# Optimization experiments

Hardware: AMD Instinct MI355X
Metric: run time of the kernel (lower is better)

The kernel has to match this reference:

```python
import jax, jax.numpy as jnp
import numpy as np

B, N, D, C, H = 8, 2048, 768, 2048, 3072
ROPE_BASE = 10000.0


def rms_norm(x, scale, eps=1e-6):
    x32 = x.astype(jnp.float32)
    normed = x32 * jax.lax.rsqrt(jnp.mean(x32 * x32, axis=-1, keepdims=True) + eps)
    return normed.astype(x.dtype) * scale


def apply_rope(x, pos):
    # x: [..., T, D], pos: [..., T] int. Half-split (llama-style) rotary embedding.
    half = x.shape[-1] // 2
    inv_freq = 1.0 / (ROPE_BASE ** (jnp.arange(half, dtype=jnp.float32) / half))
    ang = pos.astype(jnp.float32)[..., None] * inv_freq  # [..., T, half]
    cos, sin = jnp.cos(ang), jnp.sin(ang)
    x1, x2 = x[..., :half], x[..., half:]
    return jnp.concatenate([x1 * cos - x2 * sin, x1 * sin + x2 * cos], axis=-1)


def setup_inputs() -> dict:
    key = jax.random.key(0)
    ks = jax.random.split(key, 12)
    inp = {
        "latents": jax.random.normal(ks[0], (B, N, D), dtype=jnp.float32),
        "tau": jnp.float32(1.0),
        "residual_scaling": jnp.float32(1.0),
        "gumbel_noise_scale": jnp.float32(0.5),
        "positions": jnp.sort(jax.random.randint(ks[1], (B, max(N, C)), 0, 2048), axis=-1),
        # learned parameters (torch Linear weights stored [out, in])
        "codebook": jax.random.normal(ks[2], (C, D), dtype=jnp.float32),
        "norm_context_scale": jnp.ones((D,), jnp.float32),
        "norm_queries_scale": jnp.ones((D,), jnp.float32),
        "norm_ff_scale": jnp.ones((D,), jnp.float32),
        "Wq": jax.random.normal(ks[3], (D, D), jnp.float32) / np.sqrt(D),
        "Wk": jax.random.normal(ks[4], (D, D), jnp.float32) / np.sqrt(D),
        "Wv": jax.random.normal(ks[5], (D, D), jnp.float32) / np.sqrt(D),
        "bv": jnp.zeros((D,), jnp.float32),
        "Wc": jax.random.normal(ks[6], (D, D), jnp.float32) / np.sqrt(D),
        "W1": jax.random.normal(ks[7], (H, D), jnp.float32) / np.sqrt(D),
        "W2": jax.random.normal(ks[8], (D, H), jnp.float32) / np.sqrt(H),
        "W3": jax.random.normal(ks[9], (H, D), jnp.float32) / np.sqrt(D),
    }
    return inp


def reference(latents, tau, residual_scaling, gumbel_noise_scale, positions,
              codebook, norm_context_scale, norm_queries_scale, norm_ff_scale,
              Wq, Wk, Wv, bv, Wc, W1, W2, W3):
    scale = jnp.sqrt(jnp.float32(D))
    normed_context = rms_norm(codebook, norm_context_scale)        # [C, D]
    normed_queries = rms_norm(latents, norm_queries_scale)         # [B, N, D]

    q = jnp.einsum('bnd,ed->bne', normed_queries, Wq)              # [B, N, D]
    k = normed_context @ Wk.T                                      # [C, D]
    v = normed_context @ Wv.T + bv                                 # [C, D]

    q = apply_rope(q, positions[:, :N])                            # [B, N, D]
    k = apply_rope(jnp.broadcast_to(k, (B, C, D)), positions[:, :C])  # [B, C, D]

    log_alpha = jnp.einsum('bnd,bcd->bnc', q, k) / scale           # [B, N, C]

    u = jax.random.uniform(jax.random.key(42), log_alpha.shape, dtype=jnp.float32)
    gumbel = -jnp.log(-jnp.log(u + 1e-10) + 1e-10)
    log_alpha_tau = (log_alpha + gumbel_noise_scale * gumbel) / tau
    z = jax.nn.softmax(log_alpha_tau, axis=-1)                     # [B, N, C]

    attn = jnp.einsum('bnc,cd->bnd', z, v)                         # [B, N, D]
    y = jnp.einsum('bnd,ed->bne', attn, Wc)
    attn_output = residual_scaling * latents + y

    h = rms_norm(attn_output, norm_ff_scale)
    ff = jnp.einsum('bnh,dh->bnd', jax.nn.silu(jnp.einsum('bnd,hd->bnh', h, W1)) * jnp.einsum('bnd,hd->bnh', h, W3), W2)
    codebook_output = attn_output + ff
    return (codebook_output, log_alpha, log_alpha_tau, z)
```

## Files before the change

kernel.cpp:

```cpp
#include <hip/hip_runtime.h>
#include <cstdint>
#include <cstddef>


typedef __bf16 bf16_t;
typedef __bf16 bf16x8 __attribute__((ext_vector_type(8)));
typedef float  f32x4  __attribute__((ext_vector_type(4)));
typedef float  f32x16 __attribute__((ext_vector_type(16)));

#define B_    8
#define N_    2048
#define D_    768
#define C_    2048
#define H_    3072
#define NROWS 16384

#define WQ_OFF 0
#define WK_OFF 589824
#define WV_OFF 1179648
#define WC_OFF 1769472
#define W1_OFF 2359296
#define W3_OFF 4718592
#define W2_OFF 7077888
#define WTOT   9437184

#define WS_W     0ull
#define WS_TRIG  18874368ull
#define WS_VCT   25165824ull
#define WS_NC    28311552ull
#define WS_NQ    31457280ull
#define WS_Z     56623104ull
#define WS_H     28311552ull
#define WS_G     157286400ull
#define WS_VB    257949696ull

#define DO_CB    0ull
#define DO_LA    50331648ull
#define DO_LAT   184549376ull
#define DO_Z     318767104ull
#define DO_QBASE 184549376ull
#define DO_KBASE (184549376ull + 50331648ull)
#define DO_QROPE (234881024ull + 6291456ull)
#define DO_KROPE (241172480ull + 25165824ull)

__device__ __forceinline__ void gl_lds16(const void* g, void* l) {
  __builtin_amdgcn_global_load_lds((__attribute__((address_space(1))) void*)(g),
                                   (__attribute__((address_space(3))) void*)(l),
                                   16, 0, 0);
}

__device__ __forceinline__ void block_sync() {
  __builtin_amdgcn_sched_barrier(0);
  asm volatile("" ::: "memory");
  __builtin_amdgcn_s_barrier();
  asm volatile("" ::: "memory");
  __builtin_amdgcn_sched_barrier(0);
}

__device__ __forceinline__ uint32_t rotl32(uint32_t v, int d) {
  return (v << d) | (v >> (32 - d));
}
__device__ __forceinline__ void tf_round(uint32_t& x0, uint32_t& x1, int r) {
  x0 += x1; x1 = rotl32(x1, r); x1 ^= x0;
}
__device__ __forceinline__ uint2 threefry2x32(uint32_t k0, uint32_t k1,
                                              uint32_t x0, uint32_t x1) {
  const uint32_t k2 = k0 ^ k1 ^ 0x1BD11BDAu;
  x0 += k0; x1 += k1;
  tf_round(x0,x1,13); tf_round(x0,x1,15); tf_round(x0,x1,26); tf_round(x0,x1,6);
  x0 += k1; x1 += k2 + 1u;
  tf_round(x0,x1,17); tf_round(x0,x1,29); tf_round(x0,x1,16); tf_round(x0,x1,24);
  x0 += k2; x1 += k0 + 2u;
  tf_round(x0,x1,13); tf_round(x0,x1,15); tf_round(x0,x1,26); tf_round(x0,x1,6);
  x0 += k0; x1 += k1 + 3u;
  tf_round(x0,x1,17); tf_round(x0,x1,29); tf_round(x0,x1,16); tf_round(x0,x1,24);
  x0 += k1; x1 += k2 + 4u;
  tf_round(x0,x1,13); tf_round(x0,x1,15); tf_round(x0,x1,26); tf_round(x0,x1,6);
  x0 += k2; x1 += k0 + 5u;
  return make_uint2(x0, x1);
}

#define SWZ(o) ((o) ^ ((((o) >> 7) & 3) << 4))

#define PHASE_MFMA_OPEN() do { \
    block_sync(); \
    asm volatile("s_waitcnt lgkmcnt(0)" ::: "memory"); \
    __builtin_amdgcn_sched_barrier(0); \
    __builtin_amdgcn_s_setprio(1); \
  } while (0)
#define PHASE_MFMA_CLOSE() do { \
    __builtin_amdgcn_s_setprio(0); \
    __builtin_amdgcn_sched_barrier(0); \
  } while (0)

#define ROWMAP32(rg, kg) (((rg) & 3) + 8 * ((rg) >> 2) + 4 * (kg))

template <int EPI>
__global__ __launch_bounds__(512, 2) void gemm8p(
    const bf16_t* __restrict__ A, const bf16_t* __restrict__ B,
    void* outp, const void* auxp, const float* sptr,
    int M, int N, int K, long sA, long sB, long sO)
{
  __shared__ bf16_t As[2][2][8192];
  __shared__ bf16_t Bs[2][2][8192];
  const int tid  = threadIdx.x;
  const int lane = tid & 63;
  const int wid  = tid >> 6;
  const int wm = wid >> 2, wn = wid & 3;
  const int l31 = lane & 31, kg = lane >> 5;

  const int lin = (blockIdx.z * gridDim.y + blockIdx.y) * gridDim.x + blockIdx.x;
  const int swzb = (lin & 7) * 64 + (lin >> 3);
  const int bz = swzb >> 6;
  const int ny = (swzb & 63) >> 3;
  const int nx = swzb & 7;

  const bf16_t* Ab = A + (size_t)bz * (size_t)sA;
  const bf16_t* Bb = B + (size_t)bz * (size_t)sB;
  const int tm = ny * 256;
  const int tn = nx * 256;
  const int nt = K >> 6;

  const bf16_t *srcA0, *srcA1, *srcB0, *srcB1;
  {
    const int d0 = wid * 1024 + lane * 16;
    const int p0 = SWZ(d0);
    srcA0 = Ab + (size_t)(tm + (p0 >> 6)) * K + ((p0 & 63) >> 1);
    srcB0 = Bb + (size_t)(tn + (p0 >> 6)) * K + ((p0 & 63) >> 1);
    const int d1 = 8192 + wid * 1024 + lane * 16;
    const int p1 = SWZ(d1);
    srcA1 = Ab + (size_t)(tm + (p1 >> 6)) * K + ((p1 & 63) >> 1);
    srcB1 = Bb + (size_t)(tn + (p1 >> 6)) * K + ((p1 & 63) >> 1);
  }
  bf16_t* dstA = &As[0][0][0] + wid * 512;
  bf16_t* dstB = &Bs[0][0][0] + wid * 512;

  int olA[4][2], olB[2][2];
  #pragma unroll
  for (int mb = 0; mb < 4; ++mb)
    #pragma unroll
    for (int u = 0; u < 2; ++u) {
      const int o = ((wm * 128 + mb * 32 + l31) << 6) + u * 32 + (kg << 4);
      olA[mb][u] = SWZ(o);
    }
  #pragma unroll
  for (int nb = 0; nb < 2; ++nb)
    #pragma unroll
    for (int u = 0; u < 2; ++u) {
      const int o = ((wn * 64 + nb * 32 + l31) << 6) + u * 32 + (kg << 4);
      olB[nb][u] = SWZ(o);
    }

#define STG_A(tile_, kk_) do { \
    const size_t ko_ = (size_t)(tile_) * 64 + (size_t)(kk_) * 32; \
    bf16_t* db_ = dstA + (((tile_) & 1) ? 16384 : 0) + ((kk_) ? 8192 : 0); \
    gl_lds16(srcA0 + ko_, db_); \
    gl_lds16(srcA1 + ko_, db_ + 4096); \
  } while (0)
#define STG_B(tile_, kk_) do { \
    const size_t ko_ = (size_t)(tile_) * 64 + (size_t)(kk_) * 32; \
    bf16_t* db_ = dstB + (((tile_) & 1) ? 16384 : 0) + ((kk_) ? 8192 : 0); \
    gl_lds16(srcB0 + ko_, db_); \
    gl_lds16(srcB1 + ko_, db_ + 4096); \
  } while (0)

  f32x16 acc[4][2] = {};

  STG_A(0, 0); STG_B(0, 0); STG_A(0, 1); STG_B(0, 1);
  STG_B(1, 0); STG_A(1, 0); STG_B(1, 1);
  asm volatile("s_waitcnt vmcnt(6)" ::: "memory");
  block_sync();

  for (int t = 0; t < nt; ++t) {
    const int s = t & 1;
    bf16x8 bfr[2][2];
    #pragma unroll
    for (int q = 0; q < 4; ++q) {
      const int kk = q >> 1, mh = q & 1;
      if (q == 0)      { if (t + 1 < nt) STG_A(t + 1, 1); }
      else if (q == 1) { if (t + 2 < nt) STG_B(t + 2, 0); }
      else if (q == 2) { if (t + 2 < nt) STG_A(t + 2, 0); }
      else             { if (t + 2 < nt) STG_B(t + 2, 1); }
      if (mh == 0) {
        const char* Bbase = (const char*)&Bs[s][kk][0];
        #pragma unroll
        for (int nb = 0; nb < 2; ++nb)
          #pragma unroll
          for (int u = 0; u < 2; ++u)
            bfr[nb][u] = *(const bf16x8*)(Bbase + olB[nb][u]);
      }
      const char* Abase = (const char*)&As[s][kk][0];
      bf16x8 af[2][2];
      #pragma unroll
      for (int j = 0; j < 2; ++j)
        #pragma unroll
        for (int u = 0; u < 2; ++u)
          af[j][u] = *(const bf16x8*)(Abase + olA[mh * 2 + j][u]);
      PHASE_MFMA_OPEN();
      #pragma unroll
      for (int u = 0; u < 2; ++u)
        #pragma unroll
        for (int j = 0; j < 2; ++j)
          #pragma unroll
          for (int nb = 0; nb < 2; ++nb)
            acc[mh * 2 + j][nb] =
              __builtin_amdgcn_mfma_f32_32x32x16_bf16(af[j][u], bfr[nb][u], acc[mh * 2 + j][nb], 0, 0, 0);
      PHASE_MFMA_CLOSE();
      if (q == 3) asm volatile("s_waitcnt vmcnt(6)" ::: "memory");
      block_sync();
    }
  }
#undef STG_A
#undef STG_B

  #pragma unroll
  for (int mb = 0; mb < 4; ++mb) {
    #pragma unroll
    for (int nb = 0; nb < 2; ++nb) {
      const int cg = tn + wn * 64 + nb * 32 + l31;
      #pragma unroll
      for (int rg = 0; rg < 16; ++rg) {
        const int r = tm + wm * 128 + mb * 32 + ROWMAP32(rg, kg);
        const float v = acc[mb][nb][rg];
        const size_t idx = (size_t)r * N + cg;
        if (EPI == 1) {
          ((float*)outp)[(size_t)bz * sO + idx] = v * 0.03608439182435161f;
        } else {
          ((float*)outp)[(size_t)bz * sO + idx] = v;
        }
      }
    }
  }
}

template <int EPI>
__global__ __launch_bounds__(512, 2) void gemm_n384(
    const bf16_t* __restrict__ A, const bf16_t* __restrict__ B,
    void* outp, const void* auxp, const float* sptr, int K)
{
  __shared__ bf16_t As[2][2][4096];
  __shared__ bf16_t Bs[2][2][12288];
  const int tid  = threadIdx.x;
  const int lane = tid & 63;
  const int wid  = tid >> 6;
  const int wm = wid >> 2, wn = wid & 3;
  const int l31 = lane & 31, kg = lane >> 5;

  const int lin = blockIdx.y * 2 + blockIdx.x;
  const int swzb = (lin & 7) * 32 + (lin >> 3);
  const int ny = swzb >> 1;
  const int nx = swzb & 1;

  const int tm = ny * 128;
  const int tn = nx * 384;
  const int nt = K >> 6;

  const bf16_t *srcA, *srcB0, *srcB1, *srcB2;
  {
    const int d = wid * 1024 + lane * 16;
    const int p = SWZ(d);
    srcA = A + (size_t)(tm + (p >> 6)) * K + ((p & 63) >> 1);
    srcB0 = B + (size_t)(tn + (p >> 6)) * K + ((p & 63) >> 1);
    const int d1 = 8192 + d, p1 = SWZ(d1);
    srcB1 = B + (size_t)(tn + (p1 >> 6)) * K + ((p1 & 63) >> 1);
    const int d2 = 16384 + d, p2 = SWZ(d2);
    srcB2 = B + (size_t)(tn + (p2 >> 6)) * K + ((p2 & 63) >> 1);
  }
  bf16_t* dstA = &As[0][0][0] + wid * 512;
  bf16_t* dstB = &Bs[0][0][0] + wid * 512;

  int olA[2][2], olB[3][2];
  #pragma unroll
  for (int mb = 0; mb < 2; ++mb)
    #pragma unroll
    for (int u = 0; u < 2; ++u) {
      const int o = ((wm * 64 + mb * 32 + l31) << 6) + u * 32 + (kg << 4);
      olA[mb][u] = SWZ(o);
    }
  #pragma unroll
  for (int nb = 0; nb < 3; ++nb)
    #pragma unroll
    for (int u = 0; u < 2; ++u) {
      const int o = ((wn * 96 + nb * 32 + l31) << 6) + u * 32 + (kg << 4);
      olB[nb][u] = SWZ(o);
    }

#define STG_A(tile_, kk_) do { \
    const size_t ko_ = (size_t)(tile_) * 64 + (size_t)(kk_) * 32; \
    gl_lds16(srcA + ko_, dstA + (((tile_) & 1) ? 8192 : 0) + ((kk_) ? 4096 : 0)); \
  } while (0)
#define STG_B(tile_, kk_) do { \
    const size_t ko_ = (size_t)(tile_) * 64 + (size_t)(kk_) * 32; \
    bf16_t* db_ = dstB + (((tile_) & 1) ? 24576 : 0) + ((kk_) ? 12288 : 0); \
    gl_lds16(srcB0 + ko_, db_); \
    gl_lds16(srcB1 + ko_, db_ + 4096); \
    gl_lds16(srcB2 + ko_, db_ + 8192); \
  } while (0)

  f32x16 acc[2][3] = {};

  STG_A(0, 0); STG_B(0, 0); STG_A(0, 1); STG_B(0, 1);
  STG_B(1, 0); STG_A(1, 0); STG_B(1, 1);
  asm volatile("s_waitcnt vmcnt(7)" ::: "memory");
  block_sync();

  for (int t = 0; t < nt; ++t) {
    const int s = t & 1;
    bf16x8 bfr[3][2];
    #pragma unroll
    for (int q = 0; q < 4; ++q) {
      const int kk = q >> 1, mh = q & 1;
      if (q == 0)      { if (t + 1 < nt) STG_A(t + 1, 1); }
      else if (q == 1) { if (t + 2 < nt) STG_B(t + 2, 0); }
      else if (q == 2) { if (t + 2 < nt) STG_A(t + 2, 0); }
      else             { if (t + 2 < nt) STG_B(t + 2, 1); }
      if (mh == 0) {
        const char* Bbase = (const char*)&Bs[s][kk][0];
        #pragma unroll
        for (int nb = 0; nb < 3; ++nb)
          #pragma unroll
          for (int u = 0; u < 2; ++u)
            bfr[nb][u] = *(const bf16x8*)(Bbase + olB[nb][u]);
      }
      const char* Abase = (const char*)&As[s][kk][0];
      bf16x8 af[2];
      #pragma unroll
      for (int u = 0; u < 2; ++u)
        af[u] = *(const bf16x8*)(Abase + olA[mh][u]);
      PHASE_MFMA_OPEN();
      #pragma unroll
      for (int u = 0; u < 2; ++u)
        #pragma unroll
        for (int nb = 0; nb < 3; ++nb)
          acc[mh][nb] =
            __builtin_amdgcn_mfma_f32_32x32x16_bf16(af[u], bfr[nb][u], acc[mh][nb], 0, 0, 0);
      PHASE_MFMA_CLOSE();
      if (q == 3) asm volatile("s_waitcnt vmcnt(7)" ::: "memory");
      block_sync();
    }
  }
#undef STG_A
#undef STG_B

  const float sval = (EPI == 5) ? sptr[0] : 0.0f;
  #pragma unroll
  for (int mb = 0; mb < 2; ++mb) {
    #pragma unroll
    for (int nb = 0; nb < 3; ++nb) {
      const int cg = tn + wn * 96 + nb * 32 + l31;
      #pragma unroll
      for (int rg = 0; rg < 16; ++rg) {
        const int r = tm + wm * 64 + mb * 32 + ROWMAP32(rg, kg);
        const float v = acc[mb][nb][rg];
        const size_t idx = (size_t)r * 768 + cg;
        if (EPI == 2) {
          ((bf16_t*)outp)[idx] = (bf16_t)v;
        } else if (EPI == 5) {
          ((float*)outp)[idx] = sval * ((const float*)auxp)[idx] + v;
        } else {
          ((float*)outp)[idx] = ((const float*)auxp)[idx] + v;
        }
      }
    }
  }
}

__global__ __launch_bounds__(512, 2) void gemm_ff13(
    const bf16_t* __restrict__ A, const bf16_t* __restrict__ B1,
    const bf16_t* __restrict__ B3, bf16_t* __restrict__ G, int K)
{
  __shared__ bf16_t As[2][2][8192];
  __shared__ bf16_t B1s[2][2][4096];
  __shared__ bf16_t B3s[2][2][4096];
  const int tid  = threadIdx.x;
  const int lane = tid & 63;
  const int wid  = tid >> 6;
  const int wm = wid >> 2, wn = wid & 3;
  const int l31 = lane & 31, kg = lane >> 5;

  const int lin = blockIdx.y * 24 + blockIdx.x;
  const int swzb = (lin & 7) * 192 + (lin >> 3);
  const int cj = swzb / 192;
  const int local = swzb - cj * 192;
  const int st = local / 24;
  const int r  = local - st * 24;
  const int nx = cj * 3 + (r % 3);
  const int ny = st * 8 + (r / 3);

  const int tm = ny * 256;
  const int tn = nx * 128;
  const int nt = K >> 6;

  const bf16_t *srcA0, *srcA1, *srcB1p, *srcB3p;
  {
    const int d0 = wid * 1024 + lane * 16;
    const int p0 = SWZ(d0);
    srcA0 = A + (size_t)(tm + (p0 >> 6)) * K + ((p0 & 63) >> 1);
    srcB1p = B1 + (size_t)(tn + (p0 >> 6)) * K + ((p0 & 63) >> 1);
    srcB3p = B3 + (size_t)(tn + (p0 >> 6)) * K + ((p0 & 63) >> 1);
    const int d1 = 8192 + d0, p1 = SWZ(d1);
    srcA1 = A + (size_t)(tm + (p1 >> 6)) * K + ((p1 & 63) >> 1);
  }
  bf16_t* dstA  = &As[0][0][0]  + wid * 512;
  bf16_t* dstB1 = &B1s[0][0][0] + wid * 512;
  bf16_t* dstB3 = &B3s[0][0][0] + wid * 512;

  int olA[4][2], olB[2];
  #pragma unroll
  for (int mb = 0; mb < 4; ++mb)
    #pragma unroll
    for (int u = 0; u < 2; ++u) {
      const int o = ((wm * 128 + mb * 32 + l31) << 6) + u * 32 + (kg << 4);
      olA[mb][u] = SWZ(o);
    }
  #pragma unroll
  for (int u = 0; u < 2; ++u) {
    const int o = ((wn * 32 + l31) << 6) + u * 32 + (kg << 4);
    olB[u] = SWZ(o);
  }

#define STG_A(tile_, kk_) do { \
    const size_t ko_ = (size_t)(tile_) * 64 + (size_t)(kk_) * 32; \
    bf16_t* db_ = dstA + (((tile_) & 1) ? 16384 : 0) + ((kk_) ? 8192 : 0); \
    gl_lds16(srcA0 + ko_, db_); \
    gl_lds16(srcA1 + ko_, db_ + 4096); \
  } while (0)
#define STG_B(tile_, kk_) do { \
    const size_t ko_ = (size_t)(tile_) * 64 + (size_t)(kk_) * 32; \
    const int ro_ = (((tile_) & 1) ? 8192 : 0) + ((kk_) ? 4096 : 0); \
    gl_lds16(srcB1p + ko_, dstB1 + ro_); \
    gl_lds16(srcB3p + ko_, dstB3 + ro_); \
  } while (0)

  f32x16 acc1[4] = {};
  f32x16 acc3[4] = {};

  STG_A(0, 0); STG_B(0, 0); STG_A(0, 1); STG_B(0, 1);
  STG_B(1, 0); STG_A(1, 0); STG_B(1, 1);
  asm volatile("s_waitcnt vmcnt(6)" ::: "memory");
  block_sync();

  for (int t = 0; t < nt; ++t) {
    const int s = t & 1;
    bf16x8 b1r[2], b3r[2];
    #pragma unroll
    for (int q = 0; q < 4; ++q) {
      const int kk = q >> 1, mh = q & 1;
      if (q == 0)      { if (t + 1 < nt) STG_A(t + 1, 1); }
      else if (q == 1) { if (t + 2 < nt) STG_B(t + 2, 0); }
      else if (q == 2) { if (t + 2 < nt) STG_A(t + 2, 0); }
      else             { if (t + 2 < nt) STG_B(t + 2, 1); }
      if (mh == 0) {
        const char* B1base = (const char*)&B1s[s][kk][0];
        const char* B3base = (const char*)&B3s[s][kk][0];
        #pragma unroll
        for (int u = 0; u < 2; ++u) {
          b1r[u] = *(const bf16x8*)(B1base + olB[u]);
          b3r[u] = *(const bf16x8*)(B3base + olB[u]);
        }
      }
      const char* Abase = (const char*)&As[s][kk][0];
      bf16x8 af[2][2];
      #pragma unroll
      for (int j = 0; j < 2; ++j)
        #pragma unroll
        for (int u = 0; u < 2; ++u)
          af[j][u] = *(const bf16x8*)(Abase + olA[mh * 2 + j][u]);
      PHASE_MFMA_OPEN();
      #pragma unroll
      for (int u = 0; u < 2; ++u)
        #pragma unroll
        for (int j = 0; j < 2; ++j) {
          acc1[mh * 2 + j] =
            __builtin_amdgcn_mfma_f32_32x32x16_bf16(af[j][u], b1r[u], acc1[mh * 2 + j], 0, 0, 0);
          acc3[mh * 2 + j] =
            __builtin_amdgcn_mfma_f32_32x32x16_bf16(af[j][u], b3r[u], acc3[mh * 2 + j], 0, 0, 0);
        }
      PHASE_MFMA_CLOSE();
      if (q == 3) asm volatile("s_waitcnt vmcnt(6)" ::: "memory");
      block_sync();
    }
  }
#undef STG_A
#undef STG_B

  #pragma unroll
  for (int mb = 0; mb < 4; ++mb) {
    const int cg = tn + wn * 32 + l31;
    #pragma unroll
    for (int rg = 0; rg < 16; ++rg) {
      const int r2 = tm + wm * 128 + mb * 32 + ROWMAP32(rg, kg);
      const float f1 = acc1[mb][rg];
      const float f3 = acc3[mb][rg];
      const float sg = f1 / (1.0f + __expf(-f1));
      G[(size_t)r2 * 3072 + cg] = (bf16_t)(sg * f3);
    }
  }
}

template <int EPI>
__global__ __launch_bounds__(256) void gemm_bt(
    const bf16_t* __restrict__ A, const bf16_t* __restrict__ B,
    void* outp, const void* auxp, int M, int N, int K)
{
  __shared__ bf16_t Asl[128 * 64];
  __shared__ bf16_t Bsl[128 * 64];
  const int tid  = threadIdx.x;
  const int lane = tid & 63;
  const int wid  = tid >> 6;
  const int tm = blockIdx.y * 128;
  const int tn = blockIdx.x * 128;
  const int row0 = (wid & 1) * 64;
  const int col0 = (wid >> 1) * 64;
  const int fr = lane & 15;
  const int fg = lane >> 4;

  f32x4 acc[4][4] = {};

  for (int k0 = 0; k0 < K; k0 += 64) {
    #pragma unroll
    for (int i = 0; i < 4; ++i) {
      const int ebase = (i * 4 + wid) * 512;
      const int e0 = ebase + lane * 8;
      const int r  = e0 >> 6;
      const int c  = e0 & 63;
      gl_lds16(A + (size_t)(tm + r) * K + (k0 + c), &Asl[ebase]);
      gl_lds16(B + (size_t)(tn + r) * K + (k0 + c), &Bsl[ebase]);
    }
    __syncthreads();

    #pragma unroll
    for (int kk = 0; kk < 2; ++kk) {
      bf16x8 af[4], bfv[4];
      #pragma unroll
      for (int m = 0; m < 4; ++m)
        af[m] = *(const bf16x8*)&Asl[(row0 + m * 16 + fr) * 64 + kk * 32 + fg * 8];
      #pragma unroll
      for (int n = 0; n < 4; ++n)
        bfv[n] = *(const bf16x8*)&Bsl[(col0 + n * 16 + fr) * 64 + kk * 32 + fg * 8];
      #pragma unroll
      for (int m = 0; m < 4; ++m) {
        #pragma unroll
        for (int n = 0; n < 4; ++n)
          acc[m][n] = __builtin_amdgcn_mfma_f32_16x16x32_bf16(af[m], bfv[n], acc[m][n], 0, 0, 0);
      }
    }
    __syncthreads();
  }

  #pragma unroll
  for (int m = 0; m < 4; ++m) {
    const int rb = row0 + m * 16 + fg * 4;
    #pragma unroll
    for (int n = 0; n < 4; ++n) {
      const int cg = tn + col0 + n * 16 + fr;
      #pragma unroll
      for (int j = 0; j < 4; ++j) {
        const int r = tm + rb + j;
        const float v = acc[m][n][j];
        if (EPI == 2) {
          ((bf16_t*)outp)[(size_t)r * N + cg] = (bf16_t)v;
        } else if (EPI == 7) {
          ((bf16_t*)outp)[(size_t)cg * M + r] = (bf16_t)v;
        } else if (EPI == 8) {
          ((bf16_t*)outp)[(size_t)r * N + cg] = (bf16_t)(v + ((const float*)auxp)[cg]);
        }
      }
    }
  }
}

__global__ __launch_bounds__(256) void rms_rows(const float* __restrict__ x,
                                                const float* __restrict__ scale,
                                                bf16_t* __restrict__ out)
{
  const int row = blockIdx.x, t = threadIdx.x;
  const float* xr = x + (size_t)row * 768;
  const float v0 = xr[t], v1 = xr[t + 256], v2 = xr[t + 512];
  float ss = v0 * v0 + v1 * v1 + v2 * v2;
  #pragma unroll
  for (int m = 32; m; m >>= 1) ss += __shfl_xor(ss, m);
  __shared__ float red[4];
  if ((t & 63) == 0) red[t >> 6] = ss;
  __syncthreads();
  const float tot = red[0] + red[1] + red[2] + red[3];
  const float inv = rsqrtf(tot / 768.0f + 1e-6f);
  bf16_t* orow = out + (size_t)row * 768;
  orow[t]       = (bf16_t)(v0 * inv * scale[t]);
  orow[t + 256] = (bf16_t)(v1 * inv * scale[t + 256]);
  orow[t + 512] = (bf16_t)(v2 * inv * scale[t + 512]);
}

__global__ __launch_bounds__(128) void trig_fill(float* __restrict__ trig)
{
  const int p = blockIdx.x, t = threadIdx.x;
  #pragma unroll
  for (int j = 0; j < 3; ++j) {
    const int i = t + j * 128;
    const float invf = expf(-(float)i * (9.210340371976184f / 384.0f));
    const float ang  = (float)p * invf;
    trig[(size_t)p * 768 + i]       = cosf(ang);
    trig[(size_t)p * 768 + 384 + i] = sinf(ang);
  }
}

__global__ __launch_bounds__(128) void rope_qk(const bf16_t* __restrict__ qsrc,
                                               const bf16_t* __restrict__ ksrc,
                                               const int* __restrict__ pos,
                                               const float* __restrict__ trig,
                                               bf16_t* __restrict__ qdst,
                                               bf16_t* __restrict__ kdst)
{
  const int bid = blockIdx.x, t = threadIdx.x;
  const bf16_t* s;
  bf16_t* d;
  int p;
  if (bid < NROWS) {
    p = pos[bid];
    s = qsrc + (size_t)bid * 768;
    d = qdst + (size_t)bid * 768;
  } else {
    const int row = bid - NROWS;
    p = pos[row];
    s = ksrc + (size_t)(row & 2047) * 768;
    d = kdst + (size_t)row * 768;
  }
  const float* tr = trig + (size_t)p * 768;
  #pragma unroll
  for (int j = 0; j < 3; ++j) {
    const int i = t + j * 128;
    const float x1 = (float)s[i], x2 = (float)s[i + 384];
    const float c = tr[i], sn = tr[i + 384];
    d[i]       = (bf16_t)(x1 * c - x2 * sn);
    d[i + 384] = (bf16_t)(x1 * sn + x2 * c);
  }
}

__global__ __launch_bounds__(256) void softmax_g(const float* __restrict__ la,
                                                 float* __restrict__ lat,
                                                 float* __restrict__ z,
                                                 bf16_t* __restrict__ zb,
                                                 const float* __restrict__ taup,
                                                 const float* __restrict__ gnsp)
{
  const int row = blockIdx.x, t = threadIdx.x;
  const float tau = taup[0], gns = gnsp[0];
  const float* lar = la + (size_t)row * 2048;
  float* latr = lat + (size_t)row * 2048;
  float* zr   = z   + (size_t)row * 2048;
  bf16_t* zbr = zb  + (size_t)row * 2048;
  const uint32_t base = (uint32_t)row * 2048u;

  float vals[8];
  float mx = -3.0e38f;
  #pragma unroll
  for (int j = 0; j < 8; ++j) {
    const int c = t + j * 256;
    const uint32_t flat = base + (uint32_t)c;
    const uint2 rr = threefry2x32(0u, 42u, 0u, flat);
    const uint32_t bits = rr.x ^ rr.y;
    const float u = __uint_as_float((bits >> 9) | 0x3f800000u) - 1.0f;
    const float gum = -__logf(-__logf(u + 1e-10f) + 1e-10f);
    const float v = (lar[c] + gns * gum) / tau;
    vals[j] = v;
    latr[c] = v;
    mx = fmaxf(mx, v);
  }
  #pragma unroll
  for (int m = 32; m; m >>= 1) mx = fmaxf(mx, __shfl_xor(mx, m));
  __shared__ float redm[4];
  if ((t & 63) == 0) redm[t >> 6] = mx;
  __syncthreads();
  mx = fmaxf(fmaxf(redm[0], redm[1]), fmaxf(redm[2], redm[3]));

  float sum = 0.0f;
  #pragma unroll
  for (int j = 0; j < 8; ++j) { vals[j] = __expf(vals[j] - mx); sum += vals[j]; }
  #pragma unroll
  for (int m = 32; m; m >>= 1) sum += __shfl_xor(sum, m);
  __shared__ float reds[4];
  if ((t & 63) == 0) reds[t >> 6] = sum;
  __syncthreads();
  sum = reds[0] + reds[1] + reds[2] + reds[3];

  const float rinv = 1.0f / sum;
  #pragma unroll
  for (int j = 0; j < 8; ++j) {
    const int c = t + j * 256;
    const float zz = vals[j] * rinv;
    zr[c]  = zz;
    zbr[c] = (bf16_t)zz;
  }
}

__global__ __launch_bounds__(256) void convert_w(
    const float* __restrict__ wq, const float* __restrict__ wk,
    const float* __restrict__ wv, const float* __restrict__ wc,
    const float* __restrict__ w1, const float* __restrict__ w3,
    const float* __restrict__ w2, bf16_t* __restrict__ dst)
{
  const int idx = blockIdx.x * 256 + threadIdx.x;
  const float* src; int off;
  if      (idx < 589824)  { src = wq; off = 0; }
  else if (idx < 1179648) { src = wk; off = 589824; }
  else if (idx < 1769472) { src = wv; off = 1179648; }
  else if (idx < 2359296) { src = wc; off = 1769472; }
  else if (idx < 4718592) { src = w1; off = 2359296; }
  else if (idx < 7077888) { src = w3; off = 4718592; }
  else                    { src = w2; off = 7077888; }
  dst[idx] = (bf16_t)src[idx - off];
}

extern "C" void kernel_launch(void* const* d_in, const int* in_sizes, int n_in,
                              void* d_out, int out_size, void* d_ws, size_t ws_size,
                              hipStream_t stream)
{
  (void)in_sizes; (void)n_in; (void)out_size; (void)ws_size;
  const float* latents   = (const float*)d_in[0];
  const float* taup      = (const float*)d_in[1];
  const float* rsp       = (const float*)d_in[2];
  const float* gnsp      = (const float*)d_in[3];
  const int*   positions = (const int*)d_in[4];
  const float* codebook  = (const float*)d_in[5];
  const float* ncs       = (const float*)d_in[6];
  const float* nqs       = (const float*)d_in[7];
  const float* nfs       = (const float*)d_in[8];
  const float* Wq = (const float*)d_in[9];
  const float* Wk = (const float*)d_in[10];
  const float* Wv = (const float*)d_in[11];
  const float* bv = (const float*)d_in[12];
  const float* Wc = (const float*)d_in[13];
  const float* W1 = (const float*)d_in[14];
  const float* W2 = (const float*)d_in[15];
  const float* W3 = (const float*)d_in[16];

  char* ws = (char*)d_ws;
  char* ob = (char*)d_out;

  bf16_t* wbf  = (bf16_t*)(ws + WS_W);
  float*  trig = (float*)(ws + WS_TRIG);
  bf16_t* vcT  = (bf16_t*)(ws + WS_VCT);
  bf16_t* nc   = (bf16_t*)(ws + WS_NC);
  bf16_t* nq   = (bf16_t*)(ws + WS_NQ);
  bf16_t* zbuf = (bf16_t*)(ws + WS_Z);
  bf16_t* hbuf = (bf16_t*)(ws + WS_H);
  bf16_t* gbuf = (bf16_t*)(ws + WS_G);
  bf16_t* vbuf = (bf16_t*)(ws + WS_VB);

  float*  out_cb  = (float*)(ob + DO_CB);
  float*  out_la  = (float*)(ob + DO_LA);
  float*  out_lat = (float*)(ob + DO_LAT);
  float*  out_z   = (float*)(ob + DO_Z);
  bf16_t* qbase   = (bf16_t*)(ob + DO_QBASE);
  bf16_t* kbase   = (bf16_t*)(ob + DO_KBASE);
  bf16_t* qrope   = (bf16_t*)(ob + DO_QROPE);
  bf16_t* krope   = (bf16_t*)(ob + DO_KROPE);

  convert_w<<<dim3(WTOT / 256), dim3(256), 0, stream>>>(Wq, Wk, Wv, Wc, W1, W3, W2, wbf);
  rms_rows<<<dim3(C_),    dim3(256), 0, stream>>>(codebook, ncs, nc);
  rms_rows<<<dim3(NROWS), dim3(256), 0, stream>>>(latents,  nqs, nq);
  trig_fill<<<dim3(2048), dim3(128), 0, stream>>>(trig);

  gemm_bt<2><<<dim3(6, 16), dim3(256), 0, stream>>>(nc,   wbf + WK_OFF, kbase, nullptr, C_, D_, D_);
  gemm_bt<8><<<dim3(6, 16), dim3(256), 0, stream>>>(nc,   wbf + WV_OFF, vbuf,  bv,      C_, D_, D_);
  gemm_bt<7><<<dim3(6, 16), dim3(256), 0, stream>>>(vbuf, wbf + WC_OFF, vcT,   nullptr, C_, D_, D_);
  gemm_n384<2><<<dim3(2, 128), dim3(512), 0, stream>>>(nq, wbf + WQ_OFF, qbase, nullptr, nullptr, D_);

  rope_qk<<<dim3(2 * NROWS), dim3(128), 0, stream>>>(qbase, kbase, positions, trig, qrope, krope);

  gemm8p<1><<<dim3(8, 8, 8), dim3(512), 0, stream>>>(qrope, krope, out_la, nullptr, nullptr,
                                                     N_, C_, D_, (long)N_ * D_, (long)C_ * D_, (long)N_ * C_);

  softmax_g<<<dim3(NROWS), dim3(256), 0, stream>>>(out_la, out_lat, out_z, zbuf, taup, gnsp);

  gemm_n384<5><<<dim3(2, 128), dim3(512), 0, stream>>>(zbuf, vcT, out_cb, latents, rsp, C_);

  rms_rows<<<dim3(NROWS), dim3(256), 0, stream>>>(out_cb, nfs, hbuf);

  gemm_ff13<<<dim3(24, 64), dim3(512), 0, stream>>>(hbuf, wbf + W1_OFF, wbf + W3_OFF, gbuf, D_);
  gemm_n384<6><<<dim3(2, 128), dim3(512), 0, stream>>>(gbuf, wbf + W2_OFF, out_cb, out_cb, nullptr, H_);
}
```

Measured before the change: 841.1 us.

## Make FF13 GEMM persistent with tile prefetch, fuse K/V GEMMs and input RMS norms

The W1/W3 feed-forward GEMM becomes a persistent kernel with 256 blocks, each walking 6 output tiles. It issues the next tile's prologue loads before running the current tile's SiLU epilogue, so the epilogue overlaps with memory traffic. The K and V projections are merged into one kernel that shares the A-tile loads, and the two input RMS-norm launches become one. Launch overhead and repeated loads drop, but the persistent grid may balance poorly across CUs and the fused KV kernel uses more registers and LDS.

```diff
diff --git a/kernel.cpp b/kernel.cpp
--- a/kernel.cpp
+++ b/kernel.cpp
@@ -377,30 +377,17 @@
   const int wid  = tid >> 6;
   const int wm = wid >> 2, wn = wid & 3;
   const int l31 = lane & 31, kg = lane >> 5;
-
-  const int lin = blockIdx.y * 24 + blockIdx.x;
-  const int swzb = (lin & 7) * 192 + (lin >> 3);
-  const int cj = swzb / 192;
-  const int local = swzb - cj * 192;
-  const int st = local / 24;
-  const int r  = local - st * 24;
-  const int nx = cj * 3 + (r % 3);
-  const int ny = st * 8 + (r / 3);
-
-  const int tm = ny * 256;
-  const int tn = nx * 128;
+  const int xj = blockIdx.x & 7;
+  const int bl = blockIdx.x >> 3;
   const int nt = K >> 6;
 
-  const bf16_t *srcA0, *srcA1, *srcB1p, *srcB3p;
-  {
-    const int d0 = wid * 1024 + lane * 16;
-    const int p0 = SWZ(d0);
-    srcA0 = A + (size_t)(tm + (p0 >> 6)) * K + ((p0 & 63) >> 1);
-    srcB1p = B1 + (size_t)(tn + (p0 >> 6)) * K + ((p0 & 63) >> 1);
-    srcB3p = B3 + (size_t)(tn + (p0 >> 6)) * K + ((p0 & 63) >> 1);
-    const int d1 = 8192 + d0, p1 = SWZ(d1);
-    srcA1 = A + (size_t)(tm + (p1 >> 6)) * K + ((p1 & 63) >> 1);
-  }
+  const int d0 = wid * 1024 + lane * 16;
+  const int p0 = SWZ(d0);
+  const int a0r = p0 >> 6, a0c = (p0 & 63) >> 1;
+  const int d1 = 8192 + d0;
+  const int p1 = SWZ(d1);
+  const int a1r = p1 >> 6, a1c = (p1 & 63) >> 1;
+
   bf16_t* dstA  = &As[0][0][0]  + wid * 512;
   bf16_t* dstB1 = &B1s[0][0][0] + wid * 512;
   bf16_t* dstB3 = &B3s[0][0][0] + wid * 512;
@@ -418,6 +405,18 @@
     const int o = ((wn * 32 + l31) << 6) + u * 32 + (kg << 4);
     olB[u] = SWZ(o);
   }
+
+  int tm, tn;
+  const bf16_t *srcA0, *srcA1, *srcB1p, *srcB3p;
+#define SET_TILE(s_) do { \
+    const int nx_ = xj * 3 + ((s_) % 3); \
+    const int ny_ = bl * 2 + ((s_) / 3); \
+    tm = ny_ * 256; tn = nx_ * 128; \
+    srcA0  = A  + (size_t)(tm + a0r) * K + a0c; \
+    srcA1  = A  + (size_t)(tm + a1r) * K + a1c; \
+    srcB1p = B1 + (size_t)(tn + a0r) * K + a0c; \
+    srcB3p = B3 + (size_t)(tn + a0r) * K + a0c; \
+  } while (0)
 
 #define STG_A(tile_, kk_) do { \
     const size_t ko_ = (size_t)(tile_) * 64 + (size_t)(kk_) * 32; \
@@ -431,69 +430,159 @@
     gl_lds16(srcB1p + ko_, dstB1 + ro_); \
     gl_lds16(srcB3p + ko_, dstB3 + ro_); \
   } while (0)
-
-  f32x16 acc1[4] = {};
-  f32x16 acc3[4] = {};
-
-  STG_A(0, 0); STG_B(0, 0); STG_A(0, 1); STG_B(0, 1);
-  STG_B(1, 0); STG_A(1, 0); STG_B(1, 1);
+#define PROLOGUE() do { \
+    STG_A(0, 0); STG_B(0, 0); STG_A(0, 1); STG_B(0, 1); \
+    STG_B(1, 0); STG_A(1, 0); STG_B(1, 1); \
+  } while (0)
+
+  SET_TILE(0);
+  PROLOGUE();
   asm volatile("s_waitcnt vmcnt(6)" ::: "memory");
   block_sync();
 
-  for (int t = 0; t < nt; ++t) {
-    const int s = t & 1;
-    bf16x8 b1r[2], b3r[2];
-    #pragma unroll
-    for (int q = 0; q < 4; ++q) {
-      const int kk = q >> 1, mh = q & 1;
-      if (q == 0)      { if (t + 1 < nt) STG_A(t + 1, 1); }
-      else if (q == 1) { if (t + 2 < nt) STG_B(t + 2, 0); }
-      else if (q == 2) { if (t + 2 < nt) STG_A(t + 2, 0); }
-      else             { if (t + 2 < nt) STG_B(t + 2, 1); }
-      if (mh == 0) {
-        const char* B1base = (const char*)&B1s[s][kk][0];
-        const char* B3base = (const char*)&B3s[s][kk][0];
+  for (int sidx = 0; sidx < 6; ++sidx) {
+    f32x16 acc1[4] = {};
+    f32x16 acc3[4] = {};
+
+    for (int t = 0; t < nt; ++t) {
+      const int s = t & 1;
+      bf16x8 b1r[2], b3r[2];
+      #pragma unroll
+      for (int q = 0; q < 4; ++q) {
+        const int kk = q >> 1, mh = q & 1;
+        if (q == 0)      { if (t + 1 < nt) STG_A(t + 1, 1); }
+        else if (q == 1) { if (t + 2 < nt) STG_B(t + 2, 0); }
+        else if (q == 2) { if (t + 2 < nt) STG_A(t + 2, 0); }
+        else             { if (t + 2 < nt) STG_B(t + 2, 1); }
+        if (mh == 0) {
+          const char* B1base = (const char*)&B1s[s][kk][0];
+          const char* B3base = (const char*)&B3s[s][kk][0];
+          #pragma unroll
+          for (int u = 0; u < 2; ++u) {
+            b1r[u] = *(const bf16x8*)(B1base + olB[u]);
+            b3r[u] = *(const bf16x8*)(B3base + olB[u]);
+          }
+        }
+        const char* Abase = (const char*)&As[s][kk][0];
+        bf16x8 af[2][2];
         #pragma unroll
-        for (int u = 0; u < 2; ++u) {
-          b1r[u] = *(const bf16x8*)(B1base + olB[u]);
-          b3r[u] = *(const bf16x8*)(B3base + olB[u]);
-        }
-      }
-      const char* Abase = (const char*)&As[s][kk][0];
-      bf16x8 af[2][2];
-      #pragma unroll
-      for (int j = 0; j < 2; ++j)
+        for (int j = 0; j < 2; ++j)
+          #pragma unroll
+          for (int u = 0; u < 2; ++u)
+            af[j][u] = *(const bf16x8*)(Abase + olA[mh * 2 + j][u]);
+        PHASE_MFMA_OPEN();
         #pragma unroll
         for (int u = 0; u < 2; ++u)
-          af[j][u] = *(const bf16x8*)(Abase + olA[mh * 2 + j][u]);
-      PHASE_MFMA_OPEN();
-      #pragma unroll
-      for (int u = 0; u < 2; ++u)
-        #pragma unroll
-        for (int j = 0; j < 2; ++j) {
-          acc1[mh * 2 + j] =
-            __builtin_amdgcn_mfma_f32_32x32x16_bf16(af[j][u], b1r[u], acc1[mh * 2 + j], 0, 0, 0);
-          acc3[mh * 2 + j] =
-            __builtin_amdgcn_mfma_f32_32x32x16_bf16(af[j][u], b3r[u], acc3[mh * 2 + j], 0, 0, 0);
-        }
-      PHASE_MFMA_CLOSE();
-      if (q == 3) asm volatile("s_waitcnt vmcnt(6)" ::: "memory");
+          #pragma unroll
+          for (int j = 0; j < 2; ++j) {
+            acc1[mh * 2 + j] =
+              __builtin_amdgcn_mfma_f32_32x32x16_bf16(af[j][u], b1r[u], acc1[mh * 2 + j], 0, 0, 0);
+            acc3[mh * 2 + j] =
+              __builtin_amdgcn_mfma_f32_32x32x16_bf16(af[j][u], b3r[u], acc3[mh * 2 + j], 0, 0, 0);
+          }
+        PHASE_MFMA_CLOSE();
+        if (q == 3) asm volatile("s_waitcnt vmcnt(6)" ::: "memory");
+        block_sync();
+      }
+    }
+
+    const int cm = tm, cn = tn;
+    if (sidx < 5) { SET_TILE(sidx + 1); PROLOGUE(); }
+
+    #pragma unroll
+    for (int mb = 0; mb < 4; ++mb) {
+      const int cg = cn + wn * 32 + l31;
+      #pragma unroll
+      for (int rg = 0; rg < 16; ++rg) {
+        const int r2 = cm + wm * 128 + mb * 32 + ROWMAP32(rg, kg);
+        const float f1 = acc1[mb][rg];
+        const float f3 = acc3[mb][rg];
+        const float sg = f1 / (1.0f + __expf(-f1));
+        G[(size_t)r2 * 3072 + cg] = (bf16_t)(sg * f3);
+      }
+    }
+
+    if (sidx < 5) {
+      asm volatile("s_waitcnt vmcnt(6)" ::: "memory");
       block_sync();
     }
   }
 #undef STG_A
 #undef STG_B
-
-  #pragma unroll
-  for (int mb = 0; mb < 4; ++mb) {
-    const int cg = tn + wn * 32 + l31;
-    #pragma unroll
-    for (int rg = 0; rg < 16; ++rg) {
-      const int r2 = tm + wm * 128 + mb * 32 + ROWMAP32(rg, kg);
-      const float f1 = acc1[mb][rg];
-      const float f3 = acc3[mb][rg];
-      const float sg = f1 / (1.0f + __expf(-f1));
-      G[(size_t)r2 * 3072 + cg] = (bf16_t)(sg * f3);
+#undef PROLOGUE
+#undef SET_TILE
+}
+
+__global__ __launch_bounds__(256) void gemm_kv(
+    const bf16_t* __restrict__ A, const bf16_t* __restrict__ Bk,
+    const bf16_t* __restrict__ Bv, bf16_t* __restrict__ kout,
+    bf16_t* __restrict__ vout, const float* __restrict__ bias,
+    int M, int N, int K)
+{
+  __shared__ bf16_t Asl[128 * 64];
+  __shared__ bf16_t Bks[128 * 64];
+  __shared__ bf16_t Bvs[128 * 64];
+  const int tid  = threadIdx.x;
+  const int lane = tid & 63;
+  const int wid  = tid >> 6;
+  const int tm = blockIdx.y * 128;
+  const int tn = blockIdx.x * 128;
+  const int row0 = (wid & 1) * 64;
+  const int col0 = (wid >> 1) * 64;
+  const int fr = lane & 15;
+  const int fg = lane >> 4;
+
+  f32x4 acck[4][4] = {};
+  f32x4 accv[4][4] = {};
+
+  for (int k0 = 0; k0 < K; k0 += 64) {
+    #pragma unroll
+    for (int i = 0; i < 4; ++i) {
+      const int ebase = (i * 4 + wid) * 512;
+      const int e0 = ebase + lane * 8;
+      const int r  = e0 >> 6;
+      const int c  = e0 & 63;
+      gl_lds16(A  + (size_t)(tm + r) * K + (k0 + c), &Asl[ebase]);
+      gl_lds16(Bk + (size_t)(tn + r) * K + (k0 + c), &Bks[ebase]);
+      gl_lds16(Bv + (size_t)(tn + r) * K + (k0 + c), &Bvs[ebase]);
+    }
+    __syncthreads();
+
+    #pragma unroll
+    for (int kk = 0; kk < 2; ++kk) {
+      bf16x8 af[4], bk[4], bv2[4];
+      #pragma unroll
+      for (int m = 0; m < 4; ++m)
+        af[m] = *(const bf16x8*)&Asl[(row0 + m * 16 + fr) * 64 + kk * 32 + fg * 8];
+      #pragma unroll
+      for (int n = 0; n < 4; ++n) {
+        bk[n]  = *(const bf16x8*)&Bks[(col0 + n * 16 + fr) * 64 + kk * 32 + fg * 8];
+        bv2[n] = *(const bf16x8*)&Bvs[(col0 + n * 16 + fr) * 64 + kk * 32 + fg * 8];
+      }
+      #pragma unroll
+      for (int m = 0; m < 4; ++m) {
+        #pragma unroll
+        for (int n = 0; n < 4; ++n) {
+          acck[m][n] = __builtin_amdgcn_mfma_f32_16x16x32_bf16(af[m], bk[n],  acck[m][n], 0, 0, 0);
+          accv[m][n] = __builtin_amdgcn_mfma_f32_16x16x32_bf16(af[m], bv2[n], accv[m][n], 0, 0, 0);
+        }
+      }
+    }
+    __syncthreads();
+  }
+
+  #pragma unroll
+  for (int m = 0; m < 4; ++m) {
+    const int rb = row0 + m * 16 + fg * 4;
+    #pragma unroll
+    for (int n = 0; n < 4; ++n) {
+      const int cg = tn + col0 + n * 16 + fr;
+      #pragma unroll
+      for (int j = 0; j < 4; ++j) {
+        const int r = tm + rb + j;
+        kout[(size_t)r * N + cg] = (bf16_t)acck[m][n][j];
+        vout[(size_t)r * N + cg] = (bf16_t)(accv[m][n][j] + bias[cg]);
+      }
     }
   }
 }
@@ -558,16 +647,43 @@
       for (int j = 0; j < 4; ++j) {
         const int r = tm + rb + j;
         const float v = acc[m][n][j];
-        if (EPI == 2) {
+        if (EPI == 7) {
+          ((bf16_t*)outp)[(size_t)cg * M + r] = (bf16_t)v;
+        } else {
           ((bf16_t*)outp)[(size_t)r * N + cg] = (bf16_t)v;
-        } else if (EPI == 7) {
-          ((bf16_t*)outp)[(size_t)cg * M + r] = (bf16_t)v;
-        } else if (EPI == 8) {
-          ((bf16_t*)outp)[(size_t)r * N + cg] = (bf16_t)(v + ((const float*)auxp)[cg]);
         }
       }
     }
   }
+}
+
+__global__ __launch_bounds__(256) void rms_all(
+    const float* __restrict__ cb, const float* __restrict__ lt,
+    const float* __restrict__ ncs, const float* __restrict__ nqs,
+    bf16_t* __restrict__ nc, bf16_t* __restrict__ nq)
+{
+  const int row = blockIdx.x, t = threadIdx.x;
+  const float* xr;
+  const float* scale;
+  bf16_t* orow;
+  if (row < 2048) {
+    xr = cb + (size_t)row * 768; scale = ncs; orow = nc + (size_t)row * 768;
+  } else {
+    const int r2 = row - 2048;
+    xr = lt + (size_t)r2 * 768; scale = nqs; orow = nq + (size_t)r2 * 768;
+  }
+  const float v0 = xr[t], v1 = xr[t + 256], v2 = xr[t + 512];
+  float ss = v0 * v0 + v1 * v1 + v2 * v2;
+  #pragma unroll
+  for (int m = 32; m; m >>= 1) ss += __shfl_xor(ss, m);
+  __shared__ float red[4];
+  if ((t & 63) == 0) red[t >> 6] = ss;
+  __syncthreads();
+  const float tot = red[0] + red[1] + red[2] + red[3];
+  const float inv = rsqrtf(tot / 768.0f + 1e-6f);
+  orow[t]       = (bf16_t)(v0 * inv * scale[t]);
+  orow[t + 256] = (bf16_t)(v1 * inv * scale[t + 256]);
+  orow[t + 512] = (bf16_t)(v2 * inv * scale[t + 512]);
 }
 
 __global__ __launch_bounds__(256) void rms_rows(const float* __restrict__ x,
@@ -757,13 +873,12 @@
   bf16_t* krope   = (bf16_t*)(ob + DO_KROPE);
 
   convert_w<<<dim3(WTOT / 256), dim3(256), 0, stream>>>(Wq, Wk, Wv, Wc, W1, W3, W2, wbf);
-  rms_rows<<<dim3(C_),    dim3(256), 0, stream>>>(codebook, ncs, nc);
-  rms_rows<<<dim3(NROWS), dim3(256), 0, stream>>>(latents,  nqs, nq);
+  rms_all<<<dim3(C_ + NROWS), dim3(256), 0, stream>>>(codebook, latents, ncs, nqs, nc, nq);
   trig_fill<<<dim3(2048), dim3(128), 0, stream>>>(trig);
 
-  gemm_bt<2><<<dim3(6, 16), dim3(256), 0, stream>>>(nc,   wbf + WK_OFF, kbase, nullptr, C_, D_, D_);
-  gemm_bt<8><<<dim3(6, 16), dim3(256), 0, stream>>>(nc,   wbf + WV_OFF, vbuf,  bv,      C_, D_, D_);
-  gemm_bt<7><<<dim3(6, 16), dim3(256), 0, stream>>>(vbuf, wbf + WC_OFF, vcT,   nullptr, C_, D_, D_);
+  gemm_kv<<<dim3(6, 16), dim3(256), 0, stream>>>(nc, wbf + WK_OFF, wbf + WV_OFF,
+                                                 kbase, vbuf, bv, C_, D_, D_);
+  gemm_bt<7><<<dim3(6, 16), dim3(256), 0, stream>>>(vbuf, wbf + WC_OFF, vcT, nullptr, C_, D_, D_);
   gemm_n384<2><<<dim3(2, 128), dim3(512), 0, stream>>>(nq, wbf + WQ_OFF, qbase, nullptr, nullptr, D_);
 
   rope_qk<<<dim3(2 * NROWS), dim3(128), 0, stream>>>(qbase, kbase, positions, trig, qrope, krope);
@@ -777,6 +892,6 @@
 
   rms_rows<<<dim3(NROWS), dim3(256), 0, stream>>>(out_cb, nfs, hbuf);
 
-  gemm_ff13<<<dim3(24, 64), dim3(512), 0, stream>>>(hbuf, wbf + W1_OFF, wbf + W3_OFF, gbuf, D_);
+  gemm_ff13<<<dim3(256), dim3(512), 0, stream>>>(hbuf, wbf + W1_OFF, wbf + W3_OFF, gbuf, D_);
   gemm_n384<6><<<dim3(2, 128), dim3(512), 0, stream>>>(gbuf, wbf + W2_OFF, out_cb, out_cb, nullptr, H_);
 }
```

Measured after the change: 846.1 us. Within noise of the previous version (+0.6%).
